# Optimization experiments

Hardware: AMD Instinct MI355X
Metric: run time of the kernel (lower is better)

## Reference

```python
import jax, jax.numpy as jnp
import numpy as np

N_NODES = 100000
N_EDGES = 1250000
N_GRAPHS = 1024
NUM_SHAPES = 16
NUM_COLORS = 16
NUM_CLASSES = 10


def setup_inputs() -> dict:
    key = jax.random.key(0)
    ks = jax.random.split(key, 16)
    x_tokens = jax.random.randint(ks[0], (N_NODES, 2), 0, NUM_SHAPES, dtype=jnp.int64) if jax.config.jax_enable_x64 else jax.random.randint(ks[0], (N_NODES, 2), 0, NUM_SHAPES, dtype=jnp.int32)
    edge_index = jax.random.randint(ks[1], (2, N_EDGES), 0, N_NODES, dtype=jnp.int32)
    batch = jnp.sort(jax.random.randint(ks[2], (N_NODES,), 0, N_GRAPHS, dtype=jnp.int32))
    def glorot(k, shape, fan_in):
        return jax.random.normal(k, shape, jnp.float32) / jnp.sqrt(jnp.float32(fan_in))
    return {
        "x_tokens": x_tokens,
        "edge_index": edge_index,
        "batch": batch,
        "shape_emb": jax.random.normal(ks[3], (NUM_SHAPES, 8), jnp.float32),
        "color_emb": jax.random.normal(ks[4], (NUM_COLORS, 8), jnp.float32),
        "lin_w": glorot(ks[5], (32, 16), 16),
        "lin_b": jnp.zeros((32,), jnp.float32),
        "conv1_wrel": glorot(ks[6], (64, 32), 32),
        "conv1_brel": jnp.zeros((64,), jnp.float32),
        "conv1_wroot": glorot(ks[7], (64, 32), 32),
        "conv2_wrel": glorot(ks[8], (64, 64), 64),
        "conv2_brel": jnp.zeros((64,), jnp.float32),
        "conv2_wroot": glorot(ks[9], (64, 64), 64),
        "cls_w": glorot(ks[10], (NUM_CLASSES, 64), 64),
        "cls_b": jnp.zeros((NUM_CLASSES,), jnp.float32),
    }


def _graph_conv(x, src, dst, w_rel, b_rel, w_root):
    # PyG GraphConv (aggr='add'): out_i = W_rel @ sum_{j->i} x_j + b_rel + W_root @ x_i
    agg = jax.ops.segment_sum(x[src], dst, num_segments=x.shape[0])  # [N, d_in]
    return agg @ w_rel.T + b_rel + x @ w_root.T


def reference(x_tokens, edge_index, batch, shape_emb, color_emb, lin_w, lin_b,
              conv1_wrel, conv1_brel, conv1_wroot,
              conv2_wrel, conv2_brel, conv2_wroot, cls_w, cls_b):
    src, dst = edge_index[0], edge_index[1]
    # embed shape/color tokens and concat -> [N, 16]
    x = jnp.concatenate([shape_emb[x_tokens[:, 0]], color_emb[x_tokens[:, 1]]], axis=1)
    x = jax.nn.relu(x @ lin_w.T + lin_b)                      # [N, 32]
    x = jax.nn.relu(_graph_conv(x, src, dst, conv1_wrel, conv1_brel, conv1_wroot))  # [N, 64]
    x = jax.nn.relu(_graph_conv(x, src, dst, conv2_wrel, conv2_brel, conv2_wroot))  # [N, 64]
    # global mean pool over graphs
    sums = jax.ops.segment_sum(x, batch, num_segments=N_GRAPHS)           # [G, 64]
    counts = jax.ops.segment_sum(jnp.ones((x.shape[0],), x.dtype), batch, num_segments=N_GRAPHS)
    pooled = sums / jnp.maximum(counts, 1.0)[:, None]
    return pooled @ cls_w.T + cls_b                            # [G, num_classes]
```

## Files before the change

kernel.cpp:

```cpp
#include <hip/hip_runtime.h>

#define N_NODES  100000
#define N_EDGES  1250000
#define N_GRAPHS 1024
#define NB2      (N_NODES / 16)
#define CAP      512
#define EMB_BLKS ((N_NODES + 255) / 256)
#define FILLB    512

typedef __attribute__((ext_vector_type(8))) short short8;
typedef __attribute__((ext_vector_type(4))) float f32x4;
union U16 { uint4 u; short8 s; };

__device__ __forceinline__ float bflo(unsigned int w) { return __uint_as_float(w << 16); }
__device__ __forceinline__ float bfhi(unsigned int w) { return __uint_as_float(w & 0xffff0000u); }
__device__ __forceinline__ unsigned short f2bf(float f) {
  unsigned int u = __float_as_uint(f);
  u = (u + 0x7fffu + ((u >> 16) & 1u)) >> 16;
  return (unsigned short)u;
}
__device__ __forceinline__ unsigned int pack2(float a, float b) {
  return (unsigned int)f2bf(a) | ((unsigned int)f2bf(b) << 16);
}

template <int DIN>
__device__ __forceinline__ void prep_body(int t, const float* __restrict__ wrel,
                                          const float* __restrict__ wroot,
                                          unsigned short* __restrict__ Bf) {
  constexpr int NKC = (2 * DIN) / 32;
  if (t >= NKC * 4 * 64) return;
  int l = t & 63;
  int ct = (t >> 6) & 3;
  int kc = t >> 8;
  int col = ct * 16 + (l & 15);
#pragma unroll
  for (int e = 0; e < 8; ++e) {
    int k = kc * 32 + ((l >> 4) << 3) + e;
    float v = (k < DIN) ? wrel[col * DIN + k] : wroot[col * DIN + (k - DIN)];
    Bf[(size_t)t * 8 + e] = f2bf(v);
  }
}

__global__ void __launch_bounds__(256)
k_front(const int* __restrict__ tok,
        const float* __restrict__ semb, const float* __restrict__ cemb,
        const float* __restrict__ lw, const float* __restrict__ lb,
        unsigned short* __restrict__ x1,
        const float* __restrict__ w1rel, const float* __restrict__ w1root,
        const float* __restrict__ w2rel, const float* __restrict__ w2root,
        unsigned short* __restrict__ Bf1, unsigned short* __restrict__ Bf2,
        const int* __restrict__ src, const int* __restrict__ dst,
        int* __restrict__ bcur, int* __restrict__ tmp) {
  const int t = threadIdx.x;
  const int bid = blockIdx.x;
  if (bid < EMB_BLKS) {
    int i = bid * 256 + t;
    if (i >= N_NODES) return;
    int s = tok[2 * i], c = tok[2 * i + 1];
    float e[16];
#pragma unroll
    for (int k = 0; k < 8; ++k) { e[k] = semb[s * 8 + k]; e[8 + k] = cemb[c * 8 + k]; }
    unsigned int w[16];
#pragma unroll
    for (int o = 0; o < 16; ++o) {
      float a0 = lb[2 * o], a1 = lb[2 * o + 1];
#pragma unroll
      for (int k = 0; k < 16; ++k) {
        a0 = fmaf(e[k], lw[(2 * o) * 16 + k], a0);
        a1 = fmaf(e[k], lw[(2 * o + 1) * 16 + k], a1);
      }
      w[o] = pack2(fmaxf(a0, 0.f), fmaxf(a1, 0.f));
    }
    uint4* d4 = (uint4*)(x1 + (size_t)i * 32);
#pragma unroll
    for (int q = 0; q < 4; ++q)
      d4[q] = make_uint4(w[4 * q], w[4 * q + 1], w[4 * q + 2], w[4 * q + 3]);
  } else if (bid < EMB_BLKS + 6) {
    int pb = bid - EMB_BLKS;
    if (pb < 2) prep_body<32>(pb * 256 + t, w1rel, w1root, Bf1);
    else prep_body<64>((pb - 2) * 256 + t, w2rel, w2root, Bf2);
  } else {
    const int blk = bid - EMB_BLKS - 6;
    const int per = (N_EDGES + FILLB - 1) / FILLB;
    const int start = blk * per;
    const int end = min(start + per, N_EDGES);
    for (int e = start + t; e < end; e += 256) {
      int d = dst[e];
      int b = d >> 4;
      int pos = atomicAdd(&bcur[b * 16], 1);
      if (pos < CAP) tmp[(size_t)b * CAP + pos] = (src[e] << 4) | (d & 15);
    }
  }
}

template <int DIN>
__global__ void __launch_bounds__(256)
k_conv(const int* __restrict__ bcur, const int* __restrict__ tmp,
       const unsigned short* __restrict__ X,
       const uint4* __restrict__ Bf,
       const float* __restrict__ bias,
       unsigned short* __restrict__ Y) {
  constexpr int NKC = (2 * DIN) / 32;
  constexpr int LPGu = DIN / 4;
  constexpr int GROUPS = 64 / LPGu;
  __shared__ int lsrc[CAP];
  __shared__ int hdeg[16], hbase[16], hcur[16];
  __shared__ unsigned short aggT[(DIN / 8) * 16 * 8];
  const int t = threadIdx.x;
  const int lane = t & 63;
  const int wv = t >> 6;
  const int b = blockIdx.x;
  const int cnt = min(bcur[b * 16], CAP);
  if (t < 16) hdeg[t] = 0;
  __syncthreads();
  int w0 = -1, w1 = -1;
  if (t < cnt)       { w0 = tmp[(size_t)b * CAP + t];        atomicAdd(&hdeg[w0 & 15], 1); }
  if (t + 256 < cnt) { w1 = tmp[(size_t)b * CAP + t + 256];  atomicAdd(&hdeg[w1 & 15], 1); }
  __syncthreads();
  if (t == 0) {
    int run = 0;
#pragma unroll
    for (int n = 0; n < 16; ++n) { hbase[n] = run; hcur[n] = run; run += hdeg[n]; }
  }
  __syncthreads();
  if (w0 >= 0) lsrc[atomicAdd(&hcur[w0 & 15], 1)] = w0 >> 4;
  if (w1 >= 0) lsrc[atomicAdd(&hcur[w1 & 15], 1)] = w1 >> 4;
  __syncthreads();

  const int sub = lane / LPGu;
  const int lg = lane % LPGu;
#pragma unroll
  for (int k = 0; k < 4; ++k) {
    const int n = wv * 4 + k;
    const int deg = hdeg[n];
    const int base = hbase[n];
    float a0 = 0.f, a1 = 0.f, a2 = 0.f, a3 = 0.f;
    for (int j = 0; j < deg; j += 2 * GROUPS) {
      int e0 = j + sub, e1 = j + GROUPS + sub;
      int s0 = lsrc[base + min(e0, deg - 1)];
      int s1 = lsrc[base + min(e1, deg - 1)];
      uint2 r0 = *((const uint2*)(X + (size_t)s0 * DIN) + lg);
      uint2 r1 = *((const uint2*)(X + (size_t)s1 * DIN) + lg);
      if (e0 < deg) { a0 += bflo(r0.x); a1 += bfhi(r0.x); a2 += bflo(r0.y); a3 += bfhi(r0.y); }
      if (e1 < deg) { a0 += bflo(r1.x); a1 += bfhi(r1.x); a2 += bflo(r1.y); a3 += bfhi(r1.y); }
    }
#pragma unroll
    for (int off = LPGu; off < 64; off <<= 1) {
      a0 += __shfl_xor(a0, off);
      a1 += __shfl_xor(a1, off);
      a2 += __shfl_xor(a2, off);
      a3 += __shfl_xor(a3, off);
    }
    if (sub == 0) {
      uint2 w; w.x = pack2(a0, a1); w.y = pack2(a2, a3);
      *(uint2*)&aggT[(((lg >> 1) * 16 + n) << 3) + ((lg & 1) << 2)] = w;
    }
  }
  __syncthreads();

  short8 bf[NKC];
#pragma unroll
  for (int kc = 0; kc < NKC; ++kc) { U16 u; u.u = Bf[(kc * 4 + wv) * 64 + lane]; bf[kc] = u.s; }
  const float bc = bias[wv * 16 + (lane & 15)];
  const int r = lane & 15;
  const int gg = b * 16 + r;
  short8 a[NKC];
#pragma unroll
  for (int kc = 0; kc < NKC / 2; ++kc) {
    const int chunk = kc * 4 + (lane >> 4);
    U16 u; u.u = *(const uint4*)&aggT[(chunk * 16 + r) << 3];
    a[kc] = u.s;
  }
#pragma unroll
  for (int kc = NKC / 2; kc < NKC; ++kc) {
    const int colx = (kc - NKC / 2) * 32 + ((lane >> 4) << 3);
    U16 u; u.u = *(const uint4*)(X + (size_t)gg * DIN + colx);
    a[kc] = u.s;
  }
  f32x4 acc = {bc, bc, bc, bc};
#pragma unroll
  for (int kc = 0; kc < NKC; ++kc)
    acc = __builtin_amdgcn_mfma_f32_16x16x32_bf16(a[kc], bf[kc], acc, 0, 0, 0);
  const int col = wv * 16 + (lane & 15);
#pragma unroll
  for (int j = 0; j < 4; ++j) {
    int grow = b * 16 + ((lane >> 4) << 2) + j;
    Y[(size_t)grow * 64 + col] = f2bf(fmaxf(acc[j], 0.f));
  }
}

__global__ void __launch_bounds__(256)
k_pool(const unsigned short* __restrict__ y2,
       const int* __restrict__ batch,
       const float* __restrict__ cw, const float* __restrict__ cb,
       float* __restrict__ out) {
  __shared__ float part[4][64];
  const int g = blockIdx.x;
  const int lane = threadIdx.x & 63;
  const int wv = threadIdx.x >> 6;
  int lo = 0, hi = N_NODES;
  while (lo < hi) { int m = (lo + hi) >> 1; if (batch[m] < g) lo = m + 1; else hi = m; }
  int lo2 = lo, hi2 = N_NODES;
  while (lo2 < hi2) { int m = (lo2 + hi2) >> 1; if (batch[m] < g + 1) lo2 = m + 1; else hi2 = m; }
  float s = 0.f;
  for (int r = lo + wv; r < lo2; r += 4)
    s += __uint_as_float((unsigned int)y2[(size_t)r * 64 + lane] << 16);
  part[wv][lane] = s;
  __syncthreads();
  if (wv == 0) {
    float p = part[0][lane] + part[1][lane] + part[2][lane] + part[3][lane];
    int c_ = lo2 - lo;
    p *= 1.f / (float)(c_ > 0 ? c_ : 1);
    for (int c = 0; c < 10; ++c) {
      float v = p * cw[c * 64 + lane];
#pragma unroll
      for (int off = 1; off < 64; off <<= 1) v += __shfl_xor(v, off);
      if (lane == 0) out[g * 10 + c] = v + cb[c];
    }
  }
}

extern "C" void kernel_launch(void* const* d_in, const int* in_sizes, int n_in,
                              void* d_out, int out_size, void* d_ws, size_t ws_size,
                              hipStream_t stream) {
  const int*   tok    = (const int*)d_in[0];
  const int*   eidx   = (const int*)d_in[1];
  const int*   batch  = (const int*)d_in[2];
  const float* semb   = (const float*)d_in[3];
  const float* cemb   = (const float*)d_in[4];
  const float* lw     = (const float*)d_in[5];
  const float* lb     = (const float*)d_in[6];
  const float* w1rel  = (const float*)d_in[7];
  const float* b1     = (const float*)d_in[8];
  const float* w1root = (const float*)d_in[9];
  const float* w2rel  = (const float*)d_in[10];
  const float* b2     = (const float*)d_in[11];
  const float* w2root = (const float*)d_in[12];
  const float* cw     = (const float*)d_in[13];
  const float* cb     = (const float*)d_in[14];
  const int* src = eidx;
  const int* dst = eidx + N_EDGES;

  char* p = (char*)d_ws;
  unsigned short* X1 = (unsigned short*)p;  p += (size_t)N_NODES * 32 * 2;
  unsigned short* X2 = (unsigned short*)p;  p += (size_t)N_NODES * 64 * 2;
  unsigned short* Y2 = (unsigned short*)p;  p += (size_t)N_NODES * 64 * 2;
  int*   tmp  = (int*)p;  p += (size_t)NB2 * CAP * 4;
  int*   bcur = (int*)p;  p += (size_t)NB2 * 64;
  unsigned short* Bf1 = (unsigned short*)p;  p += 512 * 8 * 2;
  unsigned short* Bf2 = (unsigned short*)p;  p += 1024 * 8 * 2;

  hipMemsetAsync(bcur, 0, (size_t)NB2 * 64, stream);

  k_front<<<EMB_BLKS + 6 + FILLB, 256, 0, stream>>>(
      tok, semb, cemb, lw, lb, X1,
      w1rel, w1root, w2rel, w2root, Bf1, Bf2,
      src, dst, bcur, tmp);

  k_conv<32><<<NB2, 256, 0, stream>>>(bcur, tmp, X1, (const uint4*)Bf1, b1, X2);
  k_conv<64><<<NB2, 256, 0, stream>>>(bcur, tmp, X2, (const uint4*)Bf2, b2, Y2);

  k_pool<<<N_GRAPHS, 256, 0, stream>>>(Y2, batch, cw, cb, (float*)d_out);
}
```

Baseline: 149.7 us.

## Replace global-atomic edge bucketing with histogram-scan counting sort into 128-node buckets

Edge bucketing no longer uses global atomics into fixed-capacity 16-node slots. It now runs a deterministic counting sort: per-block shared histograms, a column scan, a bucket scan, then a fill pass writing a compact edge array. Conv blocks now each cover 128 nodes in 8 MFMA sub-tiles, with a larger shared edge list. This removes global atomic contention and the memset, at the cost of three extra launches, only 100 fill blocks of parallelism, and fewer conv blocks, each doing more serial work.

```diff
diff --git a/kernel.cpp b/kernel.cpp
--- a/kernel.cpp
+++ b/kernel.cpp
@@ -3,10 +3,11 @@
 #define N_NODES  100000
 #define N_EDGES  1250000
 #define N_GRAPHS 1024
-#define NB2      (N_NODES / 16)
-#define CAP      512
+#define NB       ((N_NODES + 127) >> 7)
+#define NBLK_F   100
+#define EPB      (N_EDGES / NBLK_F)
 #define EMB_BLKS ((N_NODES + 255) / 256)
-#define FILLB    512
+#define ECAP     3072
 
 typedef __attribute__((ext_vector_type(8))) short short8;
 typedef __attribute__((ext_vector_type(4))) float f32x4;
@@ -49,8 +50,8 @@
         const float* __restrict__ w1rel, const float* __restrict__ w1root,
         const float* __restrict__ w2rel, const float* __restrict__ w2root,
         unsigned short* __restrict__ Bf1, unsigned short* __restrict__ Bf2,
-        const int* __restrict__ src, const int* __restrict__ dst,
-        int* __restrict__ bcur, int* __restrict__ tmp) {
+        const int* __restrict__ dst, int* __restrict__ hist) {
+  __shared__ int lh[NB];
   const int t = threadIdx.x;
   const int bid = blockIdx.x;
   if (bid < EMB_BLKS) {
@@ -81,21 +82,72 @@
     else prep_body<64>((pb - 2) * 256 + t, w2rel, w2root, Bf2);
   } else {
     const int blk = bid - EMB_BLKS - 6;
-    const int per = (N_EDGES + FILLB - 1) / FILLB;
-    const int start = blk * per;
-    const int end = min(start + per, N_EDGES);
-    for (int e = start + t; e < end; e += 256) {
-      int d = dst[e];
-      int b = d >> 4;
-      int pos = atomicAdd(&bcur[b * 16], 1);
-      if (pos < CAP) tmp[(size_t)b * CAP + pos] = (src[e] << 4) | (d & 15);
-    }
+    for (int i = t; i < NB; i += 256) lh[i] = 0;
+    __syncthreads();
+    const int start = blk * EPB;
+    for (int e = start + t; e < start + EPB; e += 256)
+      atomicAdd(&lh[dst[e] >> 7], 1);
+    __syncthreads();
+    for (int i = t; i < NB; i += 256)
+      hist[i * NBLK_F + blk] = lh[i];
+  }
+}
+
+__global__ void __launch_bounds__(128)
+k_colscan(int* __restrict__ hist, int* __restrict__ btotal) {
+  __shared__ int sc[128];
+  const int b = blockIdx.x;
+  const int t = threadIdx.x;
+  int v = (t < NBLK_F) ? hist[b * NBLK_F + t] : 0;
+  sc[t] = v;
+  __syncthreads();
+  for (int off = 1; off < 128; off <<= 1) {
+    int x = (t >= off) ? sc[t - off] : 0;
+    __syncthreads();
+    sc[t] += x;
+    __syncthreads();
+  }
+  if (t < NBLK_F) hist[b * NBLK_F + t] = sc[t] - v;
+  if (t == 127) btotal[b] = sc[127];
+}
+
+__global__ void k_bscan(const int* __restrict__ btotal, int* __restrict__ bbase) {
+  __shared__ int s[1024];
+  int t = threadIdx.x;
+  int d = (t < NB) ? btotal[t] : 0;
+  s[t] = d;
+  __syncthreads();
+  for (int off = 1; off < 1024; off <<= 1) {
+    int v = (t >= off) ? s[t - off] : 0;
+    __syncthreads();
+    s[t] += v;
+    __syncthreads();
+  }
+  if (t < NB) bbase[t] = s[t] - d;
+}
+
+__global__ void __launch_bounds__(256)
+k_bfill(const int* __restrict__ src, const int* __restrict__ dst,
+        const int* __restrict__ bbase, const int* __restrict__ hist,
+        int* __restrict__ tmp) {
+  __shared__ int cur[NB];
+  const int t = threadIdx.x;
+  const int blk = blockIdx.x;
+  for (int i = t; i < NB; i += 256)
+    cur[i] = bbase[i] + hist[i * NBLK_F + blk];
+  __syncthreads();
+  const int start = blk * EPB;
+  for (int e = start + t; e < start + EPB; e += 256) {
+    int d = dst[e];
+    int pos = atomicAdd(&cur[d >> 7], 1);
+    tmp[pos] = (src[e] << 7) | (d & 127);
   }
 }
 
 template <int DIN>
 __global__ void __launch_bounds__(256)
-k_conv(const int* __restrict__ bcur, const int* __restrict__ tmp,
+k_conv(const int* __restrict__ bbase, const int* __restrict__ btotal,
+       const int* __restrict__ tmp,
        const unsigned short* __restrict__ X,
        const uint4* __restrict__ Bf,
        const float* __restrict__ bias,
@@ -103,89 +155,107 @@
   constexpr int NKC = (2 * DIN) / 32;
   constexpr int LPGu = DIN / 4;
   constexpr int GROUPS = 64 / LPGu;
-  __shared__ int lsrc[CAP];
-  __shared__ int hdeg[16], hbase[16], hcur[16];
+  __shared__ int lsrc[ECAP];
+  __shared__ int hdeg[128], hbase[128], hcur[128];
   __shared__ unsigned short aggT[(DIN / 8) * 16 * 8];
   const int t = threadIdx.x;
   const int lane = t & 63;
   const int wv = t >> 6;
   const int b = blockIdx.x;
-  const int cnt = min(bcur[b * 16], CAP);
-  if (t < 16) hdeg[t] = 0;
-  __syncthreads();
-  int w0 = -1, w1 = -1;
-  if (t < cnt)       { w0 = tmp[(size_t)b * CAP + t];        atomicAdd(&hdeg[w0 & 15], 1); }
-  if (t + 256 < cnt) { w1 = tmp[(size_t)b * CAP + t + 256];  atomicAdd(&hdeg[w1 & 15], 1); }
-  __syncthreads();
-  if (t == 0) {
-    int run = 0;
-#pragma unroll
-    for (int n = 0; n < 16; ++n) { hbase[n] = run; hcur[n] = run; run += hdeg[n]; }
-  }
-  __syncthreads();
-  if (w0 >= 0) lsrc[atomicAdd(&hcur[w0 & 15], 1)] = w0 >> 4;
-  if (w1 >= 0) lsrc[atomicAdd(&hcur[w1 & 15], 1)] = w1 >> 4;
-  __syncthreads();
-
+  const int base = bbase[b];
+  const int cnt = min(btotal[b], ECAP);
+
+  if (t < 128) hdeg[t] = 0;
+  __syncthreads();
+  for (int i = t; i < cnt; i += 256) atomicAdd(&hdeg[tmp[base + i] & 127], 1);
+  __syncthreads();
+  {
+    int d = (t < 128) ? hdeg[t] : 0;
+    if (t < 128) hbase[t] = d;
+    __syncthreads();
+    for (int off = 1; off < 128; off <<= 1) {
+      int v = 0;
+      if (t < 128 && t >= off) v = hbase[t - off];
+      __syncthreads();
+      if (t < 128) hbase[t] += v;
+      __syncthreads();
+    }
+    if (t < 128) { int excl = hbase[t] - d; hbase[t] = excl; hcur[t] = excl; }
+  }
+  __syncthreads();
+  for (int i = t; i < cnt; i += 256) {
+    int w = tmp[base + i];
+    lsrc[atomicAdd(&hcur[w & 127], 1)] = w >> 7;
+  }
+  __syncthreads();
+
+  short8 bf[NKC];
+#pragma unroll
+  for (int kc = 0; kc < NKC; ++kc) { U16 u; u.u = Bf[(kc * 4 + wv) * 64 + lane]; bf[kc] = u.s; }
+  const float bc = bias[wv * 16 + (lane & 15)];
   const int sub = lane / LPGu;
   const int lg = lane % LPGu;
-#pragma unroll
-  for (int k = 0; k < 4; ++k) {
-    const int n = wv * 4 + k;
-    const int deg = hdeg[n];
-    const int base = hbase[n];
-    float a0 = 0.f, a1 = 0.f, a2 = 0.f, a3 = 0.f;
-    for (int j = 0; j < deg; j += 2 * GROUPS) {
-      int e0 = j + sub, e1 = j + GROUPS + sub;
-      int s0 = lsrc[base + min(e0, deg - 1)];
-      int s1 = lsrc[base + min(e1, deg - 1)];
-      uint2 r0 = *((const uint2*)(X + (size_t)s0 * DIN) + lg);
-      uint2 r1 = *((const uint2*)(X + (size_t)s1 * DIN) + lg);
-      if (e0 < deg) { a0 += bflo(r0.x); a1 += bfhi(r0.x); a2 += bflo(r0.y); a3 += bfhi(r0.y); }
-      if (e1 < deg) { a0 += bflo(r1.x); a1 += bfhi(r1.x); a2 += bflo(r1.y); a3 += bfhi(r1.y); }
-    }
-#pragma unroll
-    for (int off = LPGu; off < 64; off <<= 1) {
-      a0 += __shfl_xor(a0, off);
-      a1 += __shfl_xor(a1, off);
-      a2 += __shfl_xor(a2, off);
-      a3 += __shfl_xor(a3, off);
-    }
-    if (sub == 0) {
-      uint2 w; w.x = pack2(a0, a1); w.y = pack2(a2, a3);
-      *(uint2*)&aggT[(((lg >> 1) * 16 + n) << 3) + ((lg & 1) << 2)] = w;
-    }
-  }
-  __syncthreads();
-
-  short8 bf[NKC];
-#pragma unroll
-  for (int kc = 0; kc < NKC; ++kc) { U16 u; u.u = Bf[(kc * 4 + wv) * 64 + lane]; bf[kc] = u.s; }
-  const float bc = bias[wv * 16 + (lane & 15)];
-  const int r = lane & 15;
-  const int gg = b * 16 + r;
-  short8 a[NKC];
-#pragma unroll
-  for (int kc = 0; kc < NKC / 2; ++kc) {
-    const int chunk = kc * 4 + (lane >> 4);
-    U16 u; u.u = *(const uint4*)&aggT[(chunk * 16 + r) << 3];
-    a[kc] = u.s;
-  }
-#pragma unroll
-  for (int kc = NKC / 2; kc < NKC; ++kc) {
-    const int colx = (kc - NKC / 2) * 32 + ((lane >> 4) << 3);
-    U16 u; u.u = *(const uint4*)(X + (size_t)gg * DIN + colx);
-    a[kc] = u.s;
-  }
-  f32x4 acc = {bc, bc, bc, bc};
-#pragma unroll
-  for (int kc = 0; kc < NKC; ++kc)
-    acc = __builtin_amdgcn_mfma_f32_16x16x32_bf16(a[kc], bf[kc], acc, 0, 0, 0);
-  const int col = wv * 16 + (lane & 15);
-#pragma unroll
-  for (int j = 0; j < 4; ++j) {
-    int grow = b * 16 + ((lane >> 4) << 2) + j;
-    Y[(size_t)grow * 64 + col] = f2bf(fmaxf(acc[j], 0.f));
+
+#pragma unroll
+  for (int st = 0; st < 8; ++st) {
+#pragma unroll
+    for (int k = 0; k < 4; ++k) {
+      const int r = wv * 4 + k;
+      const int n = st * 16 + r;
+      const int deg = hdeg[n];
+      const int eb = hbase[n];
+      float a0 = 0.f, a1 = 0.f, a2 = 0.f, a3 = 0.f;
+      for (int j = 0; j < deg; j += 2 * GROUPS) {
+        int e0 = j + sub, e1 = j + GROUPS + sub;
+        int s0 = lsrc[eb + min(e0, deg - 1)];
+        int s1 = lsrc[eb + min(e1, deg - 1)];
+        uint2 r0 = *((const uint2*)(X + (size_t)s0 * DIN) + lg);
+        uint2 r1 = *((const uint2*)(X + (size_t)s1 * DIN) + lg);
+        if (e0 < deg) { a0 += bflo(r0.x); a1 += bfhi(r0.x); a2 += bflo(r0.y); a3 += bfhi(r0.y); }
+        if (e1 < deg) { a0 += bflo(r1.x); a1 += bfhi(r1.x); a2 += bflo(r1.y); a3 += bfhi(r1.y); }
+      }
+#pragma unroll
+      for (int off = LPGu; off < 64; off <<= 1) {
+        a0 += __shfl_xor(a0, off);
+        a1 += __shfl_xor(a1, off);
+        a2 += __shfl_xor(a2, off);
+        a3 += __shfl_xor(a3, off);
+      }
+      if (sub == 0) {
+        uint2 w; w.x = pack2(a0, a1); w.y = pack2(a2, a3);
+        *(uint2*)&aggT[(((lg >> 1) * 16 + r) << 3) + ((lg & 1) << 2)] = w;
+      }
+    }
+    __syncthreads();
+
+    const int r = lane & 15;
+    const int gg = b * 128 + st * 16 + r;
+    const int gs = (gg < N_NODES) ? gg : 0;
+    short8 a[NKC];
+#pragma unroll
+    for (int kc = 0; kc < NKC / 2; ++kc) {
+      const int chunk = kc * 4 + (lane >> 4);
+      U16 u; u.u = *(const uint4*)&aggT[(chunk * 16 + r) << 3];
+      a[kc] = u.s;
+    }
+#pragma unroll
+    for (int kc = NKC / 2; kc < NKC; ++kc) {
+      const int colx = (kc - NKC / 2) * 32 + ((lane >> 4) << 3);
+      U16 u; u.u = *(const uint4*)(X + (size_t)gs * DIN + colx);
+      a[kc] = u.s;
+    }
+    f32x4 acc = {bc, bc, bc, bc};
+#pragma unroll
+    for (int kc = 0; kc < NKC; ++kc)
+      acc = __builtin_amdgcn_mfma_f32_16x16x32_bf16(a[kc], bf[kc], acc, 0, 0, 0);
+    const int col = wv * 16 + (lane & 15);
+#pragma unroll
+    for (int j = 0; j < 4; ++j) {
+      int grow = b * 128 + st * 16 + ((lane >> 4) << 2) + j;
+      if (grow < N_NODES)
+        Y[(size_t)grow * 64 + col] = f2bf(fmaxf(acc[j], 0.f));
+    }
+    __syncthreads();
   }
 }
 
@@ -245,20 +315,23 @@
   unsigned short* X1 = (unsigned short*)p;  p += (size_t)N_NODES * 32 * 2;
   unsigned short* X2 = (unsigned short*)p;  p += (size_t)N_NODES * 64 * 2;
   unsigned short* Y2 = (unsigned short*)p;  p += (size_t)N_NODES * 64 * 2;
-  int*   tmp  = (int*)p;  p += (size_t)NB2 * CAP * 4;
-  int*   bcur = (int*)p;  p += (size_t)NB2 * 64;
+  int*   tmp    = (int*)p;  p += (size_t)N_EDGES * 4;
+  int*   hist   = (int*)p;  p += (size_t)NB * NBLK_F * 4;
+  int*   btotal = (int*)p;  p += 4096;
+  int*   bbase  = (int*)p;  p += 4096;
   unsigned short* Bf1 = (unsigned short*)p;  p += 512 * 8 * 2;
   unsigned short* Bf2 = (unsigned short*)p;  p += 1024 * 8 * 2;
 
-  hipMemsetAsync(bcur, 0, (size_t)NB2 * 64, stream);
-
-  k_front<<<EMB_BLKS + 6 + FILLB, 256, 0, stream>>>(
+  k_front<<<EMB_BLKS + 6 + NBLK_F, 256, 0, stream>>>(
       tok, semb, cemb, lw, lb, X1,
-      w1rel, w1root, w2rel, w2root, Bf1, Bf2,
-      src, dst, bcur, tmp);
-
-  k_conv<32><<<NB2, 256, 0, stream>>>(bcur, tmp, X1, (const uint4*)Bf1, b1, X2);
-  k_conv<64><<<NB2, 256, 0, stream>>>(bcur, tmp, X2, (const uint4*)Bf2, b2, Y2);
+      w1rel, w1root, w2rel, w2root, Bf1, Bf2, dst, hist);
+
+  k_colscan<<<NB, 128, 0, stream>>>(hist, btotal);
+  k_bscan<<<1, 1024, 0, stream>>>(btotal, bbase);
+  k_bfill<<<NBLK_F, 256, 0, stream>>>(src, dst, bbase, hist, tmp);
+
+  k_conv<32><<<NB, 256, 0, stream>>>(bbase, btotal, tmp, X1, (const uint4*)Bf1, b1, X2);
+  k_conv<64><<<NB, 256, 0, stream>>>(bbase, btotal, tmp, X2, (const uint4*)Bf2, b2, Y2);
 
   k_pool<<<N_GRAPHS, 256, 0, stream>>>(Y2, batch, cw, cb, (float*)d_out);
 }
```

Measured after the change: 181.2 us. +21.0%, slower.
